# Performance work log

Measured on AMD Instinct MI355X. Metric: run time of the kernel, lower is better.

Reference implementation:

```python
import jax, jax.numpy as jnp
import numpy as np

V, E, HL, HC, B = 32000, 256, 1024, 256, 512


def setup_inputs() -> dict:
    key = jax.random.key(0)
    ks = jax.random.split(key, 10)
    s = 0.05  # small init scale, like uniform(-init_range, init_range)
    return {
        "lang_h0": jax.random.normal(ks[0], (B, HL), jnp.float32) * s,
        "ctx_h": jax.random.normal(ks[1], (B, HC), jnp.float32) * s,
        "word_emb": jax.random.normal(ks[2], (V, E), jnp.float32) * s,
        "dec_W": jax.random.normal(ks[3], (E, HL), jnp.float32) * s,
        "dec_b": jax.random.normal(ks[4], (E,), jnp.float32) * s,
        "w_ih": jax.random.normal(ks[5], (3 * HL, E + HC), jnp.float32) * s,
        "w_hh": jax.random.normal(ks[6], (3 * HL, HL), jnp.float32) * s,
        "b_ih": jax.random.normal(ks[7], (3 * HL,), jnp.float32) * s,
        "b_hh": jax.random.normal(ks[8], (3 * HL,), jnp.float32) * s,
        "inpt0": jax.random.randint(ks[9], (B,), 0, V, jnp.int32),
        "temperature": 1,
        "max_words": 100,
    }


def _gru_cell(x, h, w_ih, w_hh, b_ih, b_hh):
    # PyTorch nn.GRUCell math. x: [B, E+HC], h: [B, HL]
    gi = x @ w_ih.T + b_ih  # [B, 3*HL]
    gh = h @ w_hh.T + b_hh
    i_r, i_z, i_n = jnp.split(gi, 3, axis=-1)
    h_r, h_z, h_n = jnp.split(gh, 3, axis=-1)
    r = jax.nn.sigmoid(i_r + h_r)
    z = jax.nn.sigmoid(i_z + h_z)
    n = jnp.tanh(i_n + r * h_n)
    return (1.0 - z) * n + z * h


def reference(lang_h0, ctx_h, word_emb, dec_W, dec_b, w_ih, w_hh, b_ih, b_hh,
              inpt0, temperature, max_words):
    temp = jnp.float32(temperature)

    def step(carry, k):
        inpt, h = carry
        x = jnp.concatenate([word_emb[inpt], ctx_h], axis=1)  # [B, E+HC]
        h = _gru_cell(x, h, w_ih, w_hh, b_ih, b_hh)           # [B, HL]
        dec = h @ dec_W.T + dec_b                              # [B, E]
        logits = (dec @ word_emb.T) / temp                     # [B, V]
        # scores.sub_(max); multinomial(exp(scores)) == categorical(logits)
        out = jax.random.categorical(k, logits, axis=-1).astype(jnp.int32)
        return (out, h), (out, h)

    keys = jax.random.split(jax.random.key(1), max_words)
    (last_out, lang_h), (outs, lang_hs) = jax.lax.scan(
        step, (inpt0, lang_h0), keys)
    # final extra writer step (as in write_batch after the loop)
    x = jnp.concatenate([word_emb[last_out], ctx_h], axis=1)
    lang_h = _gru_cell(x, lang_h, w_ih, w_hh, b_ih, b_hh)
    all_lang_hs = jnp.concatenate(
        [lang_h0[None], lang_hs, lang_h[None]], axis=0)  # [T+2, B, HL]
    return outs, all_lang_hs
```

## Files before the change

### kernel.cpp

```cpp
#include <hip/hip_runtime.h>
#include <stdint.h>
#include <limits.h>

#define T_STEPS 100
#define BSZ 512
#define HL 1024
#define HC 256
#define EMB 256
#define VOC 32000
#define NCHUNK 250

typedef __attribute__((ext_vector_type(8))) short short8;
typedef __attribute__((ext_vector_type(4))) float f32x4;
typedef __attribute__((ext_vector_type(4))) unsigned short u16x4;
#define MFMA16(a, b, c) __builtin_amdgcn_mfma_f32_16x16x32_bf16(a, b, c, 0, 0, 0)

#define ACC6(acc, ah, am, al, bh, bm, bl) \
  { acc = MFMA16(ah, bh, acc); acc = MFMA16(ah, bm, acc); acc = MFMA16(am, bh, acc); \
    acc = MFMA16(ah, bl, acc); acc = MFMA16(am, bm, acc); acc = MFMA16(al, bh, acc); }

__device__ __forceinline__ void threefry2x32(uint32_t k0, uint32_t k1,
                                             uint32_t x0, uint32_t x1,
                                             uint32_t& o0, uint32_t& o1) {
  uint32_t ks2 = k0 ^ k1 ^ 0x1BD11BDAu;
  x0 += k0; x1 += k1;
#define TF_R(x, r) (((x) << (r)) | ((x) >> (32 - (r))))
#define TF_RND(r) { x0 += x1; x1 = TF_R(x1, r); x1 ^= x0; }
  TF_RND(13) TF_RND(15) TF_RND(26) TF_RND(6)
  x0 += k1; x1 += ks2 + 1u;
  TF_RND(17) TF_RND(29) TF_RND(16) TF_RND(24)
  x0 += ks2; x1 += k0 + 2u;
  TF_RND(13) TF_RND(15) TF_RND(26) TF_RND(6)
  x0 += k0; x1 += k1 + 3u;
  TF_RND(17) TF_RND(29) TF_RND(16) TF_RND(24)
  x0 += k1; x1 += ks2 + 4u;
  TF_RND(13) TF_RND(15) TF_RND(26) TF_RND(6)
  x0 += ks2; x1 += k0 + 5u;
#undef TF_RND
#undef TF_R
  o0 = x0; o1 = x1;
}

__device__ __forceinline__ float gumbel_from_u32(uint32_t bits) {
  float f = __uint_as_float((bits >> 9) | 0x3f800000u) - 1.0f;
  f = fmaxf(f, 1.17549435e-38f);
  return -logf(-logf(f));
}

__device__ __forceinline__ float read_temp(const int* p) {
  int v = *p;
  if (v >= -(1 << 24) && v <= (1 << 24)) return (float)v;
  return __int_as_float(v);
}

__device__ __forceinline__ unsigned short f2bf(float x) {
  uint32_t u = __float_as_uint(x);
  u += 0x7fffu + ((u >> 16) & 1u);
  return (unsigned short)(u >> 16);
}
__device__ __forceinline__ float bf2f(unsigned short h) {
  return __uint_as_float(((uint32_t)h) << 16);
}
__device__ __forceinline__ void split3(float x, unsigned short& h,
                                       unsigned short& m, unsigned short& l) {
  h = f2bf(x);
  float r = x - bf2f(h);
  m = f2bf(r);
  r = r - bf2f(m);
  l = f2bf(r);
}

__global__ __launch_bounds__(256) void k_split3(const float* __restrict__ src,
                                                unsigned short* __restrict__ hi,
                                                unsigned short* __restrict__ mid,
                                                unsigned short* __restrict__ lo,
                                                int n4) {
  int i = blockIdx.x * 256 + threadIdx.x;
  if (i >= n4) return;
  float4 v = ((const float4*)src)[i];
  float vv[4] = {v.x, v.y, v.z, v.w};
  u16x4 h, m, l;
#pragma unroll
  for (int j = 0; j < 4; j++) {
    unsigned short a, b, c;
    split3(vv[j], a, b, c);
    h[j] = a; m[j] = b; l[j] = c;
  }
  ((u16x4*)hi)[i] = h;
  ((u16x4*)mid)[i] = m;
  ((u16x4*)lo)[i] = l;
}

__global__ __launch_bounds__(256) void k_init(const float* __restrict__ lang_h0,
                                              const int* __restrict__ inpt0,
                                              uint32_t* __restrict__ keys,
                                              int* __restrict__ cur_tok,
                                              float* __restrict__ H0) {
  int idx = blockIdx.x * 256 + threadIdx.x;
  if (idx < T_STEPS) {
    uint32_t o0, o1;
    threefry2x32(0u, 1u, 0u, (uint32_t)idx, o0, o1);
    keys[2 * idx] = o0; keys[2 * idx + 1] = o1;
  }
  if (idx < BSZ) cur_tok[idx] = inpt0[idx];
  if (idx < BSZ * HL) H0[idx] = lang_h0[idx];
}

__global__ __launch_bounds__(256) void k_gi(
    const float* __restrict__ emb, const float* __restrict__ ctx,
    const int* __restrict__ tok,
    const unsigned short* __restrict__ wih_h, const unsigned short* __restrict__ wih_m,
    const unsigned short* __restrict__ wih_l,
    const float* __restrict__ b_ih, float* __restrict__ GI) {
  int tid = threadIdx.x;
  int wave = tid >> 6, lane = tid & 63;
  int ml = lane & 15, quad = lane >> 4;
  int n0 = blockIdx.x * 64;
  int bA = blockIdx.y * 64 + wave * 16 + ml;
  int myt = tok[bA];
  f32x4 acc[4];
#pragma unroll
  for (int tn = 0; tn < 4; tn++) acc[tn] = (f32x4){0.f, 0.f, 0.f, 0.f};

  for (int k0 = 0; k0 < 512; k0 += 32) {
    int k = k0 + quad * 8;
    const float* src = (k < 256) ? (emb + (size_t)myt * 256 + k)
                                 : (ctx + (size_t)bA * 256 + (k - 256));
    float4 x0 = *(const float4*)src;
    float4 x1 = *(const float4*)(src + 4);
    float xf[8] = {x0.x, x0.y, x0.z, x0.w, x1.x, x1.y, x1.z, x1.w};
    short8 ah, am_, al;
#pragma unroll
    for (int j = 0; j < 8; j++) {
      unsigned short a, b, c;
      split3(xf[j], a, b, c);
      ah[j] = (short)a; am_[j] = (short)b; al[j] = (short)c;
    }
#pragma unroll
    for (int tn = 0; tn < 4; tn++) {
      int n = n0 + tn * 16 + ml;
      size_t off = (size_t)n * 512 + k;
      short8 bh = *(const short8*)(wih_h + off);
      short8 bm = *(const short8*)(wih_m + off);
      short8 bl = *(const short8*)(wih_l + off);
      ACC6(acc[tn], ah, am_, al, bh, bm, bl);
    }
  }
  int brow = blockIdx.y * 64 + wave * 16 + quad * 4;
#pragma unroll
  for (int tn = 0; tn < 4; tn++) {
    int n = n0 + tn * 16 + ml;
    float bias = b_ih[n];
#pragma unroll
    for (int reg = 0; reg < 4; reg++)
      GI[(size_t)(brow + reg) * 3072 + n] = acc[tn][reg] + bias;
  }
}

__global__ __launch_bounds__(128) void k_gru(const float* __restrict__ Hin,
                                             const float* __restrict__ w_hh,
                                             const float* __restrict__ b_hh,
                                             const float* __restrict__ GI,
                                             float* __restrict__ Hout) {
  __shared__ __align__(16) float Ah[32][68];
  __shared__ __align__(16) float Wr[32][34];
  __shared__ __align__(16) float Wz[32][34];
  __shared__ __align__(16) float Wn[32][34];
  int tid = threadIdx.x;
  int ti = tid & 15;
  int tb = tid >> 4;
  int b0 = blockIdx.y * 64, i0 = blockIdx.x * 32;
  int sr = tid >> 3;
  int kq = (tid & 7) * 4;
  float acc[3][8][2] = {};

  for (int k0 = 0; k0 < 1024; k0 += 32) {
#pragma unroll
    for (int i = 0; i < 4; i++) {
      int r = sr + 16 * i;
      float4 h4 = *(const float4*)&Hin[(size_t)(b0 + r) * 1024 + k0 + kq];
      Ah[kq + 0][r] = h4.x; Ah[kq + 1][r] = h4.y; Ah[kq + 2][r] = h4.z; Ah[kq + 3][r] = h4.w;
    }
#pragma unroll
    for (int g = 0; g < 3; g++) {
      float* Wg = (g == 0 ? &Wr[0][0] : g == 1 ? &Wz[0][0] : &Wn[0][0]);
      const float* src = w_hh + (size_t)(g * 1024 + i0) * 1024;
#pragma unroll
      for (int i = 0; i < 2; i++) {
        int r = sr + 16 * i;
        float4 w4 = *(const float4*)&src[(size_t)r * 1024 + k0 + kq];
        Wg[(kq + 0) * 34 + r] = w4.x; Wg[(kq + 1) * 34 + r] = w4.y;
        Wg[(kq + 2) * 34 + r] = w4.z; Wg[(kq + 3) * 34 + r] = w4.w;
      }
    }
    __syncthreads();
#pragma unroll
    for (int kk = 0; kk < 32; kk++) {
      float4 a0 = *(float4*)&Ah[kk][tb * 8];
      float4 a1 = *(float4*)&Ah[kk][tb * 8 + 4];
      float av[8] = {a0.x, a0.y, a0.z, a0.w, a1.x, a1.y, a1.z, a1.w};
      float2 wr2 = *(float2*)&Wr[kk][ti * 2];
      float2 wz2 = *(float2*)&Wz[kk][ti * 2];
      float2 wn2 = *(float2*)&Wn[kk][ti * 2];
      float wv0[2] = {wr2.x, wr2.y};
      float wv1[2] = {wz2.x, wz2.y};
      float wv2[2] = {wn2.x, wn2.y};
#pragma unroll
      for (int bb = 0; bb < 8; bb++)
#pragma unroll
        for (int j = 0; j < 2; j++) {
          acc[0][bb][j] += av[bb] * wv0[j];
          acc[1][bb][j] += av[bb] * wv1[j];
          acc[2][bb][j] += av[bb] * wv2[j];
        }
    }
    __syncthreads();
  }
  int i = i0 + ti * 2;
  float2 bhr = *(const float2*)&b_hh[i];
  float2 bhz = *(const float2*)&b_hh[1024 + i];
  float2 bhn = *(const float2*)&b_hh[2048 + i];
  float bhrv[2] = {bhr.x, bhr.y}, bhzv[2] = {bhz.x, bhz.y}, bhnv[2] = {bhn.x, bhn.y};
#pragma unroll
  for (int bb = 0; bb < 8; bb++) {
    int b = b0 + tb * 8 + bb;
    float2 gir = *(const float2*)&GI[(size_t)b * 3072 + i];
    float2 giz = *(const float2*)&GI[(size_t)b * 3072 + 1024 + i];
    float2 gin = *(const float2*)&GI[(size_t)b * 3072 + 2048 + i];
    float2 h2 = *(const float2*)&Hin[(size_t)b * 1024 + i];
    float girv[2] = {gir.x, gir.y}, gizv[2] = {giz.x, giz.y}, ginv[2] = {gin.x, gin.y};
    float hv[2] = {h2.x, h2.y}, ov[2];
#pragma unroll
    for (int j = 0; j < 2; j++) {
      float r = 1.0f / (1.0f + expf(-(girv[j] + acc[0][bb][j] + bhrv[j])));
      float z = 1.0f / (1.0f + expf(-(gizv[j] + acc[1][bb][j] + bhzv[j])));
      float n = tanhf(ginv[j] + r * (acc[2][bb][j] + bhnv[j]));
      ov[j] = (1.0f - z) * n + z * hv[j];
    }
    float2 o; o.x = ov[0]; o.y = ov[1];
    *(float2*)&Hout[(size_t)b * 1024 + i] = o;
  }
}

__global__ __launch_bounds__(256) void k_dec(const float* __restrict__ H,
                                             const float* __restrict__ dec_W,
                                             const float* __restrict__ dec_b,
                                             unsigned short* __restrict__ dh,
                                             unsigned short* __restrict__ dm,
                                             unsigned short* __restrict__ dl) {
  __shared__ __align__(16) float As[32][20];
  __shared__ __align__(16) float Ws[32][68];
  int tid = threadIdx.x;
  int tb = tid >> 4;
  int tv = tid & 15;
  int col0 = blockIdx.x * 64, row0 = blockIdx.y * 16;
  int srw = tid >> 3;
  int kq = (tid & 7) * 4;
  float acc[4] = {};
  for (int k0 = 0; k0 < 1024; k0 += 32) {
    if (srw < 16) {
      float4 a4 = *(const float4*)&H[(size_t)(row0 + srw) * 1024 + k0 + kq];
      As[kq + 0][srw] = a4.x; As[kq + 1][srw] = a4.y; As[kq + 2][srw] = a4.z; As[kq + 3][srw] = a4.w;
    }
#pragma unroll
    for (int i = 0; i < 2; i++) {
      int r = srw + 32 * i;
      float4 w4 = *(const float4*)&dec_W[(size_t)(col0 + r) * 1024 + k0 + kq];
      Ws[kq + 0][r] = w4.x; Ws[kq + 1][r] = w4.y;
      Ws[kq + 2][r] = w4.z; Ws[kq + 3][r] = w4.w;
    }
    __syncthreads();
#pragma unroll
    for (int kk = 0; kk < 32; kk++) {
      float a = As[kk][tb];
      float4 w = *(float4*)&Ws[kk][tv * 4];
      float wv[4] = {w.x, w.y, w.z, w.w};
#pragma unroll
      for (int j = 0; j < 4; j++) acc[j] += a * wv[j];
    }
    __syncthreads();
  }
  int col = col0 + tv * 4;
  float4 b4 = *(const float4*)&dec_b[col];
  float bv[4] = {b4.x, b4.y, b4.z, b4.w};
  u16x4 h, m, l;
#pragma unroll
  for (int j = 0; j < 4; j++) {
    unsigned short a, b, c;
    split3(acc[j] + bv[j], a, b, c);
    h[j] = a; m[j] = b; l[j] = c;
  }
  size_t o = (size_t)(row0 + tb) * 256 + col;
  *(u16x4*)(dh + o) = h;
  *(u16x4*)(dm + o) = m;
  *(u16x4*)(dl + o) = l;
}

__global__ __launch_bounds__(256) void k_logits(const unsigned short* __restrict__ dh,
                                                const unsigned short* __restrict__ dm,
                                                const unsigned short* __restrict__ dl,
                                                const unsigned short* __restrict__ ebh,
                                                const unsigned short* __restrict__ ebm,
                                                const unsigned short* __restrict__ ebl,
                                                const uint32_t* __restrict__ keys,
                                                int t,
                                                const int* __restrict__ temp_ptr,
                                                float* __restrict__ pval,
                                                int* __restrict__ pidx) {
  __shared__ __align__(16) unsigned short Eh[128 * 40];
  __shared__ __align__(16) unsigned short Em[128 * 40];
  __shared__ __align__(16) unsigned short El[128 * 40];
  int tid = threadIdx.x;
  int wave = tid >> 6, lane = tid & 63;
  int ml = lane & 15, quad = lane >> 4;
  int c = blockIdx.x;
  int v0 = c * 128;
  int b0 = blockIdx.y * 128;
  f32x4 acc[2][8];
#pragma unroll
  for (int mi = 0; mi < 2; mi++)
#pragma unroll
    for (int tv = 0; tv < 8; tv++) acc[mi][tv] = (f32x4){0.f, 0.f, 0.f, 0.f};

  for (int k0 = 0; k0 < 256; k0 += 32) {
    __syncthreads();
#pragma unroll
    for (int i = 0; i < 4; i++) {
      int idx4 = tid + i * 256;
      int v = idx4 >> 3;
      int k4 = (idx4 & 7) * 4;
      size_t go = (size_t)(v0 + v) * 256 + k0 + k4;
      *(u16x4*)&Eh[v * 40 + k4] = *(const u16x4*)(ebh + go);
      *(u16x4*)&Em[v * 40 + k4] = *(const u16x4*)(ebm + go);
      *(u16x4*)&El[v * 40 + k4] = *(const u16x4*)(ebl + go);
    }
    __syncthreads();
    short8 ah[2], am_[2], al[2];
#pragma unroll
    for (int mi = 0; mi < 2; mi++) {
      int brow = b0 + wave * 32 + mi * 16 + ml;
      size_t off = (size_t)brow * 256 + k0 + quad * 8;
      ah[mi] = *(const short8*)(dh + off);
      am_[mi] = *(const short8*)(dm + off);
      al[mi] = *(const short8*)(dl + off);
    }
#pragma unroll
    for (int tv = 0; tv < 8; tv++) {
      int lo = (tv * 16 + ml) * 40 + quad * 8;
      short8 bh = *(const short8*)&Eh[lo];
      short8 bm = *(const short8*)&Em[lo];
      short8 bl = *(const short8*)&El[lo];
#pragma unroll
      for (int mi = 0; mi < 2; mi++)
        ACC6(acc[mi][tv], ah[mi], am_[mi], al[mi], bh, bm, bl);
    }
  }
  float temp = read_temp(temp_ptr);
  uint32_t kk0 = keys[2 * t], kk1 = keys[2 * t + 1];
#pragma unroll
  for (int mi = 0; mi < 2; mi++) {
    float best[4];
    int bidx[4];
#pragma unroll
    for (int reg = 0; reg < 4; reg++) { best[reg] = -3.402823466e38f; bidx[reg] = INT_MAX; }
#pragma unroll
    for (int tv = 0; tv < 8; tv++) {
      int v = v0 + tv * 16 + ml;
#pragma unroll
      for (int reg = 0; reg < 4; reg++) {
        int b = b0 + wave * 32 + mi * 16 + quad * 4 + reg;
        uint32_t o0, o1;
        threefry2x32(kk0, kk1, 0u, (uint32_t)(b * VOC + v), o0, o1);
        float s = acc[mi][tv][reg] / temp + gumbel_from_u32(o0 ^ o1);
        if (s > best[reg]) { best[reg] = s; bidx[reg] = v; }
      }
    }
#pragma unroll
    for (int off = 1; off < 16; off <<= 1) {
#pragma unroll
      for (int reg = 0; reg < 4; reg++) {
        float ov = __shfl_xor(best[reg], off, 64);
        int oi = __shfl_xor(bidx[reg], off, 64);
        if (ov > best[reg] || (ov == best[reg] && oi < bidx[reg])) {
          best[reg] = ov; bidx[reg] = oi;
        }
      }
    }
    if (ml == 0) {
#pragma unroll
      for (int reg = 0; reg < 4; reg++) {
        int b = b0 + wave * 32 + mi * 16 + quad * 4 + reg;
        pval[(size_t)b * NCHUNK + c] = best[reg];
        pidx[(size_t)b * NCHUNK + c] = bidx[reg];
      }
    }
  }
}

__global__ __launch_bounds__(256) void k_argmax_final(const float* __restrict__ pval,
                                                      const int* __restrict__ pidx,
                                                      int* __restrict__ cur_tok,
                                                      float* __restrict__ outs_t) {
  __shared__ float sv[256];
  __shared__ int si[256];
  int b = blockIdx.x, tid = threadIdx.x;
  float bv = -3.402823466e38f;
  int bi = INT_MAX;
  for (int c = tid; c < NCHUNK; c += 256) {
    float v = pval[(size_t)b * NCHUNK + c];
    int i2 = pidx[(size_t)b * NCHUNK + c];
    if (v > bv || (v == bv && i2 < bi)) { bv = v; bi = i2; }
  }
  sv[tid] = bv; si[tid] = bi;
  __syncthreads();
  for (int s = 128; s > 0; s >>= 1) {
    if (tid < s) {
      float v = sv[tid + s]; int i2 = si[tid + s];
      if (v > sv[tid] || (v == sv[tid] && i2 < si[tid])) { sv[tid] = v; si[tid] = i2; }
    }
    __syncthreads();
  }
  if (tid == 0) { cur_tok[b] = si[0]; outs_t[b] = (float)si[0]; }
}

extern "C" void kernel_launch(void* const* d_in, const int* in_sizes, int n_in,
                              void* d_out, int out_size, void* d_ws, size_t ws_size,
                              hipStream_t stream) {
  const float* lang_h0 = (const float*)d_in[0];
  const float* ctx_h   = (const float*)d_in[1];
  const float* emb     = (const float*)d_in[2];
  const float* dec_W   = (const float*)d_in[3];
  const float* dec_b   = (const float*)d_in[4];
  const float* w_ih    = (const float*)d_in[5];
  const float* w_hh    = (const float*)d_in[6];
  const float* b_ih    = (const float*)d_in[7];
  const float* b_hh    = (const float*)d_in[8];
  const int*   inpt0   = (const int*)d_in[9];
  const int*   temp_p  = (const int*)d_in[10];

  float* out = (float*)d_out;
  float* outs = out;
  float* Hbase = out + (size_t)T_STEPS * BSZ;

  uint8_t* ws = (uint8_t*)d_ws;
  uint32_t* keys = (uint32_t*)ws;
  int* cur_tok = (int*)(ws + 4096);
  unsigned short* dh = (unsigned short*)(ws + 8192);
  unsigned short* dm = dh + (size_t)BSZ * EMB;
  unsigned short* dl = dm + (size_t)BSZ * EMB;
  float* pval = (float*)(dl + (size_t)BSZ * EMB);
  int* pidx = (int*)(pval + (size_t)BSZ * NCHUNK);
  float* GI = (float*)(pidx + (size_t)BSZ * NCHUNK);
  unsigned short* wih_h = (unsigned short*)(GI + (size_t)BSZ * 3 * HL);
  unsigned short* wih_m = wih_h + (size_t)3 * HL * 512;
  unsigned short* wih_l = wih_m + (size_t)3 * HL * 512;
  unsigned short* ebh = wih_l + (size_t)3 * HL * 512;
  unsigned short* ebm = ebh + (size_t)VOC * EMB;
  unsigned short* ebl = ebm + (size_t)VOC * EMB;

  k_split3<<<(3 * HL * 512 / 4 + 255) / 256, 256, 0, stream>>>(w_ih, wih_h, wih_m, wih_l,
                                                               3 * HL * 512 / 4);
  k_split3<<<(VOC * EMB / 4 + 255) / 256, 256, 0, stream>>>(emb, ebh, ebm, ebl,
                                                            VOC * EMB / 4);
  k_init<<<(BSZ * HL) / 256, 256, 0, stream>>>(lang_h0, inpt0, keys, cur_tok, Hbase);

  for (int t = 0; t <= T_STEPS; t++) {
    const float* Hin = Hbase + (size_t)t * BSZ * HL;
    float* Hout = Hbase + (size_t)(t + 1) * BSZ * HL;
    k_gi<<<dim3(48, 8), 256, 0, stream>>>(emb, ctx_h, cur_tok,
                                          wih_h, wih_m, wih_l, b_ih, GI);
    k_gru<<<dim3(32, 8), 128, 0, stream>>>(Hin, w_hh, b_hh, GI, Hout);
    if (t == T_STEPS) break;
    k_dec<<<dim3(4, 32), 256, 0, stream>>>(Hout, dec_W, dec_b, dh, dm, dl);
    k_logits<<<dim3(NCHUNK, 4), 256, 0, stream>>>(dh, dm, dl, ebh, ebm, ebl, keys, t,
                                                  temp_p, pval, pidx);
    k_argmax_final<<<BSZ, 256, 0, stream>>>(pval, pidx, cur_tok, outs + (size_t)t * BSZ);
  }
}
```

Baseline: 29.09 ms.

## Fuse GRU input and hidden GEMMs into one split-bf16 MFMA GEMM

Concatenates w_ih and w_hh into one pre-split bf16x3 weight matrix with a separate column block for the hidden n-gate. The recurrent h@w_hh GEMM then runs on MFMA instead of the scalar FP32 shared-memory kernel. Each step now pre-splits [emb|ctx|h] into bf16 triples, runs one combined GEMM that skips zero K ranges per gate, and applies the gates in a separate pointwise kernel. This adds workspace, an extra launch and a global round-trip for the gate preactivations, and it relies on 3-way bf16 splitting to keep FP32-like accuracy.

```diff
diff --git a/kernel.cpp b/kernel.cpp
--- a/kernel.cpp
+++ b/kernel.cpp
@@ -9,6 +9,8 @@
 #define EMB 256
 #define VOC 32000
 #define NCHUNK 250
+#define KCAT 1536
+#define NCAT 4096
 
 typedef __attribute__((ext_vector_type(8))) short short8;
 typedef __attribute__((ext_vector_type(4))) float f32x4;
@@ -91,11 +93,48 @@
   ((u16x4*)lo)[i] = l;
 }
 
+__global__ __launch_bounds__(256) void k_wprep(const float* __restrict__ w_ih,
+                                               const float* __restrict__ w_hh,
+                                               unsigned short* __restrict__ wch,
+                                               unsigned short* __restrict__ wcm,
+                                               unsigned short* __restrict__ wcl) {
+  int i4 = blockIdx.x * 256 + threadIdx.x;
+  if (i4 >= NCAT * KCAT / 4) return;
+  int idx = i4 * 4;
+  int n = idx / KCAT;
+  int k = idx - n * KCAT;
+  float4 v;
+  if (k < 512) {
+    if (n < 3072) v = *(const float4*)&w_ih[(size_t)n * 512 + k];
+    else          v = (float4){0.f, 0.f, 0.f, 0.f};
+  } else {
+    int g = n >> 10;
+    if (g < 2)       v = *(const float4*)&w_hh[(size_t)n * 1024 + (k - 512)];
+    else if (g == 3) v = *(const float4*)&w_hh[(size_t)(n - 1024) * 1024 + (k - 512)];
+    else             v = (float4){0.f, 0.f, 0.f, 0.f};
+  }
+  float vv[4] = {v.x, v.y, v.z, v.w};
+  u16x4 h, m, l;
+#pragma unroll
+  for (int j = 0; j < 4; j++) {
+    unsigned short a, b, c;
+    split3(vv[j], a, b, c);
+    h[j] = a; m[j] = b; l[j] = c;
+  }
+  size_t o = (size_t)n * KCAT + k;
+  *(u16x4*)(wch + o) = h;
+  *(u16x4*)(wcm + o) = m;
+  *(u16x4*)(wcl + o) = l;
+}
+
 __global__ __launch_bounds__(256) void k_init(const float* __restrict__ lang_h0,
                                               const int* __restrict__ inpt0,
+                                              const float* __restrict__ b_ih,
+                                              const float* __restrict__ b_hh,
                                               uint32_t* __restrict__ keys,
                                               int* __restrict__ cur_tok,
-                                              float* __restrict__ H0) {
+                                              float* __restrict__ H0,
+                                              float* __restrict__ bc) {
   int idx = blockIdx.x * 256 + threadIdx.x;
   if (idx < T_STEPS) {
     uint32_t o0, o1;
@@ -103,46 +142,79 @@
     keys[2 * idx] = o0; keys[2 * idx + 1] = o1;
   }
   if (idx < BSZ) cur_tok[idx] = inpt0[idx];
+  if (idx < NCAT) {
+    int g = idx >> 10;
+    float v;
+    if (g < 2)       v = b_ih[idx] + b_hh[idx];
+    else if (g == 2) v = b_ih[idx];
+    else             v = b_hh[idx - 1024];
+    bc[idx] = v;
+  }
   if (idx < BSZ * HL) H0[idx] = lang_h0[idx];
 }
 
-__global__ __launch_bounds__(256) void k_gi(
-    const float* __restrict__ emb, const float* __restrict__ ctx,
-    const int* __restrict__ tok,
-    const unsigned short* __restrict__ wih_h, const unsigned short* __restrict__ wih_m,
-    const unsigned short* __restrict__ wih_l,
-    const float* __restrict__ b_ih, float* __restrict__ GI) {
+__global__ __launch_bounds__(256) void k_xsplit(const float* __restrict__ emb,
+                                                const float* __restrict__ ctx,
+                                                const int* __restrict__ tok,
+                                                const float* __restrict__ Hin,
+                                                unsigned short* __restrict__ xh,
+                                                unsigned short* __restrict__ xm,
+                                                unsigned short* __restrict__ xl) {
+  int i4 = blockIdx.x * 256 + threadIdx.x;
+  if (i4 >= BSZ * KCAT / 4) return;
+  int idx = i4 * 4;
+  int b = idx / KCAT;
+  int k = idx - b * KCAT;
+  const float* src;
+  if (k < 256)      src = emb + (size_t)tok[b] * 256 + k;
+  else if (k < 512) src = ctx + (size_t)b * 256 + (k - 256);
+  else              src = Hin + (size_t)b * 1024 + (k - 512);
+  float4 v = *(const float4*)src;
+  float vv[4] = {v.x, v.y, v.z, v.w};
+  u16x4 h, m, l;
+#pragma unroll
+  for (int j = 0; j < 4; j++) {
+    unsigned short a, bb, c;
+    split3(vv[j], a, bb, c);
+    h[j] = a; m[j] = bb; l[j] = c;
+  }
+  size_t o = (size_t)b * KCAT + k;
+  *(u16x4*)(xh + o) = h;
+  *(u16x4*)(xm + o) = m;
+  *(u16x4*)(xl + o) = l;
+}
+
+__global__ __launch_bounds__(256) void k_big(
+    const unsigned short* __restrict__ xh, const unsigned short* __restrict__ xm,
+    const unsigned short* __restrict__ xl,
+    const unsigned short* __restrict__ wch, const unsigned short* __restrict__ wcm,
+    const unsigned short* __restrict__ wcl,
+    const float* __restrict__ bc, float* __restrict__ Gp) {
   int tid = threadIdx.x;
   int wave = tid >> 6, lane = tid & 63;
   int ml = lane & 15, quad = lane >> 4;
   int n0 = blockIdx.x * 64;
+  int gate = n0 >> 10;
+  int kbeg = (gate == 3) ? 512 : 0;
+  int kend = (gate == 2) ? 512 : KCAT;
   int bA = blockIdx.y * 64 + wave * 16 + ml;
-  int myt = tok[bA];
   f32x4 acc[4];
 #pragma unroll
   for (int tn = 0; tn < 4; tn++) acc[tn] = (f32x4){0.f, 0.f, 0.f, 0.f};
 
-  for (int k0 = 0; k0 < 512; k0 += 32) {
+  for (int k0 = kbeg; k0 < kend; k0 += 32) {
     int k = k0 + quad * 8;
-    const float* src = (k < 256) ? (emb + (size_t)myt * 256 + k)
-                                 : (ctx + (size_t)bA * 256 + (k - 256));
-    float4 x0 = *(const float4*)src;
-    float4 x1 = *(const float4*)(src + 4);
-    float xf[8] = {x0.x, x0.y, x0.z, x0.w, x1.x, x1.y, x1.z, x1.w};
-    short8 ah, am_, al;
-#pragma unroll
-    for (int j = 0; j < 8; j++) {
-      unsigned short a, b, c;
-      split3(xf[j], a, b, c);
-      ah[j] = (short)a; am_[j] = (short)b; al[j] = (short)c;
-    }
+    size_t aoff = (size_t)bA * KCAT + k;
+    short8 ah = *(const short8*)(xh + aoff);
+    short8 am_ = *(const short8*)(xm + aoff);
+    short8 al = *(const short8*)(xl + aoff);
 #pragma unroll
     for (int tn = 0; tn < 4; tn++) {
       int n = n0 + tn * 16 + ml;
-      size_t off = (size_t)n * 512 + k;
-      short8 bh = *(const short8*)(wih_h + off);
-      short8 bm = *(const short8*)(wih_m + off);
-      short8 bl = *(const short8*)(wih_l + off);
+      size_t off = (size_t)n * KCAT + k;
+      short8 bh = *(const short8*)(wch + off);
+      short8 bm = *(const short8*)(wcm + off);
+      short8 bl = *(const short8*)(wcl + off);
       ACC6(acc[tn], ah, am_, al, bh, bm, bl);
     }
   }
@@ -150,96 +222,41 @@
 #pragma unroll
   for (int tn = 0; tn < 4; tn++) {
     int n = n0 + tn * 16 + ml;
-    float bias = b_ih[n];
+    float bias = bc[n];
 #pragma unroll
     for (int reg = 0; reg < 4; reg++)
-      GI[(size_t)(brow + reg) * 3072 + n] = acc[tn][reg] + bias;
-  }
-}
-
-__global__ __launch_bounds__(128) void k_gru(const float* __restrict__ Hin,
-                                             const float* __restrict__ w_hh,
-                                             const float* __restrict__ b_hh,
-                                             const float* __restrict__ GI,
-                                             float* __restrict__ Hout) {
-  __shared__ __align__(16) float Ah[32][68];
-  __shared__ __align__(16) float Wr[32][34];
-  __shared__ __align__(16) float Wz[32][34];
-  __shared__ __align__(16) float Wn[32][34];
-  int tid = threadIdx.x;
-  int ti = tid & 15;
-  int tb = tid >> 4;
-  int b0 = blockIdx.y * 64, i0 = blockIdx.x * 32;
-  int sr = tid >> 3;
-  int kq = (tid & 7) * 4;
-  float acc[3][8][2] = {};
-
-  for (int k0 = 0; k0 < 1024; k0 += 32) {
-#pragma unroll
-    for (int i = 0; i < 4; i++) {
-      int r = sr + 16 * i;
-      float4 h4 = *(const float4*)&Hin[(size_t)(b0 + r) * 1024 + k0 + kq];
-      Ah[kq + 0][r] = h4.x; Ah[kq + 1][r] = h4.y; Ah[kq + 2][r] = h4.z; Ah[kq + 3][r] = h4.w;
-    }
-#pragma unroll
-    for (int g = 0; g < 3; g++) {
-      float* Wg = (g == 0 ? &Wr[0][0] : g == 1 ? &Wz[0][0] : &Wn[0][0]);
-      const float* src = w_hh + (size_t)(g * 1024 + i0) * 1024;
-#pragma unroll
-      for (int i = 0; i < 2; i++) {
-        int r = sr + 16 * i;
-        float4 w4 = *(const float4*)&src[(size_t)r * 1024 + k0 + kq];
-        Wg[(kq + 0) * 34 + r] = w4.x; Wg[(kq + 1) * 34 + r] = w4.y;
-        Wg[(kq + 2) * 34 + r] = w4.z; Wg[(kq + 3) * 34 + r] = w4.w;
-      }
-    }
-    __syncthreads();
-#pragma unroll
-    for (int kk = 0; kk < 32; kk++) {
-      float4 a0 = *(float4*)&Ah[kk][tb * 8];
-      float4 a1 = *(float4*)&Ah[kk][tb * 8 + 4];
-      float av[8] = {a0.x, a0.y, a0.z, a0.w, a1.x, a1.y, a1.z, a1.w};
-      float2 wr2 = *(float2*)&Wr[kk][ti * 2];
-      float2 wz2 = *(float2*)&Wz[kk][ti * 2];
-      float2 wn2 = *(float2*)&Wn[kk][ti * 2];
-      float wv0[2] = {wr2.x, wr2.y};
-      float wv1[2] = {wz2.x, wz2.y};
-      float wv2[2] = {wn2.x, wn2.y};
-#pragma unroll
-      for (int bb = 0; bb < 8; bb++)
-#pragma unroll
-        for (int j = 0; j < 2; j++) {
-          acc[0][bb][j] += av[bb] * wv0[j];
-          acc[1][bb][j] += av[bb] * wv1[j];
-          acc[2][bb][j] += av[bb] * wv2[j];
-        }
-    }
-    __syncthreads();
-  }
-  int i = i0 + ti * 2;
-  float2 bhr = *(const float2*)&b_hh[i];
-  float2 bhz = *(const float2*)&b_hh[1024 + i];
-  float2 bhn = *(const float2*)&b_hh[2048 + i];
-  float bhrv[2] = {bhr.x, bhr.y}, bhzv[2] = {bhz.x, bhz.y}, bhnv[2] = {bhn.x, bhn.y};
-#pragma unroll
-  for (int bb = 0; bb < 8; bb++) {
-    int b = b0 + tb * 8 + bb;
-    float2 gir = *(const float2*)&GI[(size_t)b * 3072 + i];
-    float2 giz = *(const float2*)&GI[(size_t)b * 3072 + 1024 + i];
-    float2 gin = *(const float2*)&GI[(size_t)b * 3072 + 2048 + i];
-    float2 h2 = *(const float2*)&Hin[(size_t)b * 1024 + i];
-    float girv[2] = {gir.x, gir.y}, gizv[2] = {giz.x, giz.y}, ginv[2] = {gin.x, gin.y};
-    float hv[2] = {h2.x, h2.y}, ov[2];
-#pragma unroll
-    for (int j = 0; j < 2; j++) {
-      float r = 1.0f / (1.0f + expf(-(girv[j] + acc[0][bb][j] + bhrv[j])));
-      float z = 1.0f / (1.0f + expf(-(gizv[j] + acc[1][bb][j] + bhzv[j])));
-      float n = tanhf(ginv[j] + r * (acc[2][bb][j] + bhnv[j]));
-      ov[j] = (1.0f - z) * n + z * hv[j];
-    }
-    float2 o; o.x = ov[0]; o.y = ov[1];
-    *(float2*)&Hout[(size_t)b * 1024 + i] = o;
-  }
+      Gp[(size_t)(brow + reg) * NCAT + n] = acc[tn][reg] + bias;
+  }
+}
+
+__global__ __launch_bounds__(256) void k_point(const float* __restrict__ Gp,
+                                               const float* __restrict__ Hin,
+                                               float* __restrict__ Hout) {
+  int i4 = blockIdx.x * 256 + threadIdx.x;
+  if (i4 >= BSZ * HL / 4) return;
+  int idx = i4 * 4;
+  int b = idx >> 10, i = idx & 1023;
+  const float* g = Gp + (size_t)b * NCAT;
+  float4 gr = *(const float4*)(g + i);
+  float4 gz = *(const float4*)(g + 1024 + i);
+  float4 gn = *(const float4*)(g + 2048 + i);
+  float4 gh = *(const float4*)(g + 3072 + i);
+  float4 h4 = *(const float4*)(Hin + (size_t)b * 1024 + i);
+  float grv[4] = {gr.x, gr.y, gr.z, gr.w};
+  float gzv[4] = {gz.x, gz.y, gz.z, gz.w};
+  float gnv[4] = {gn.x, gn.y, gn.z, gn.w};
+  float ghv[4] = {gh.x, gh.y, gh.z, gh.w};
+  float hv[4] = {h4.x, h4.y, h4.z, h4.w};
+  float ov[4];
+#pragma unroll
+  for (int j = 0; j < 4; j++) {
+    float r = 1.0f / (1.0f + expf(-grv[j]));
+    float z = 1.0f / (1.0f + expf(-gzv[j]));
+    float n = tanhf(gnv[j] + r * ghv[j]);
+    ov[j] = (1.0f - z) * n + z * hv[j];
+  }
+  float4 o; o.x = ov[0]; o.y = ov[1]; o.z = ov[2]; o.w = ov[3];
+  *(float4*)&Hout[(size_t)b * 1024 + i] = o;
 }
 
 __global__ __launch_bounds__(256) void k_dec(const float* __restrict__ H,
@@ -450,26 +467,32 @@
   unsigned short* dl = dm + (size_t)BSZ * EMB;
   float* pval = (float*)(dl + (size_t)BSZ * EMB);
   int* pidx = (int*)(pval + (size_t)BSZ * NCHUNK);
-  float* GI = (float*)(pidx + (size_t)BSZ * NCHUNK);
-  unsigned short* wih_h = (unsigned short*)(GI + (size_t)BSZ * 3 * HL);
-  unsigned short* wih_m = wih_h + (size_t)3 * HL * 512;
-  unsigned short* wih_l = wih_m + (size_t)3 * HL * 512;
-  unsigned short* ebh = wih_l + (size_t)3 * HL * 512;
+  float* Gp = (float*)(pidx + (size_t)BSZ * NCHUNK);
+  unsigned short* xh = (unsigned short*)(Gp + (size_t)BSZ * NCAT);
+  unsigned short* xm = xh + (size_t)BSZ * KCAT;
+  unsigned short* xl = xm + (size_t)BSZ * KCAT;
+  unsigned short* wch = xl + (size_t)BSZ * KCAT;
+  unsigned short* wcm = wch + (size_t)NCAT * KCAT;
+  unsigned short* wcl = wcm + (size_t)NCAT * KCAT;
+  float* bc = (float*)(wcl + (size_t)NCAT * KCAT);
+  unsigned short* ebh = (unsigned short*)(bc + NCAT);
   unsigned short* ebm = ebh + (size_t)VOC * EMB;
   unsigned short* ebl = ebm + (size_t)VOC * EMB;
 
-  k_split3<<<(3 * HL * 512 / 4 + 255) / 256, 256, 0, stream>>>(w_ih, wih_h, wih_m, wih_l,
-                                                               3 * HL * 512 / 4);
+  k_wprep<<<(NCAT * KCAT / 4 + 255) / 256, 256, 0, stream>>>(w_ih, w_hh, wch, wcm, wcl);
   k_split3<<<(VOC * EMB / 4 + 255) / 256, 256, 0, stream>>>(emb, ebh, ebm, ebl,
                                                             VOC * EMB / 4);
-  k_init<<<(BSZ * HL) / 256, 256, 0, stream>>>(lang_h0, inpt0, keys, cur_tok, Hbase);
+  k_init<<<(BSZ * HL) / 256, 256, 0, stream>>>(lang_h0, inpt0, b_ih, b_hh,
+                                               keys, cur_tok, Hbase, bc);
 
   for (int t = 0; t <= T_STEPS; t++) {
     const float* Hin = Hbase + (size_t)t * BSZ * HL;
     float* Hout = Hbase + (size_t)(t + 1) * BSZ * HL;
-    k_gi<<<dim3(48, 8), 256, 0, stream>>>(emb, ctx_h, cur_tok,
-                                          wih_h, wih_m, wih_l, b_ih, GI);
-    k_gru<<<dim3(32, 8), 128, 0, stream>>>(Hin, w_hh, b_hh, GI, Hout);
+    k_xsplit<<<(BSZ * KCAT / 4 + 255) / 256, 256, 0, stream>>>(emb, ctx_h, cur_tok,
+                                                               Hin, xh, xm, xl);
+    k_big<<<dim3(NCAT / 64, BSZ / 64), 256, 0, stream>>>(xh, xm, xl, wch, wcm, wcl,
+                                                         bc, Gp);
+    k_point<<<(BSZ * HL / 4 + 255) / 256, 256, 0, stream>>>(Gp, Hin, Hout);
     if (t == T_STEPS) break;
     k_dec<<<dim3(4, 32), 256, 0, stream>>>(Hout, dec_W, dec_b, dh, dm, dl);
     k_logits<<<dim3(NCHUNK, 4), 256, 0, stream>>>(dh, dm, dl, ebh, ebm, ebl, keys, t,
```

Result: slower. 31.24 ms (+7.4%).

## Fuse argmax into logits via packed atomicMax, presplit embeddings, retile GRU

Applied to the files above, without the earlier changes.

Removes the per-step argmax reduction kernel. Each logits block now folds its chunk maximum into a packed 64-bit key with atomicMax, and the next gi kernel unpacks the token and writes it to the output. The gi kernel also reads the pre-split bf16 embedding and context tables (context is split once up front) instead of splitting on the fly. The GRU kernel is retiled to 32 batch rows per block to double the block count. This saves a launch and the partial-buffer traffic per step, at the cost of atomic contention and an extra write in the decoder kernel to reset the packed keys.

```diff
diff --git a/kernel.cpp b/kernel.cpp
--- a/kernel.cpp
+++ b/kernel.cpp
@@ -70,6 +70,10 @@
   l = f2bf(r);
 }
 
+__device__ __forceinline__ int unpack_tok(unsigned long long pk) {
+  return (int)(0xFFFFFFFFu - (uint32_t)(pk & 0xFFFFFFFFull));
+}
+
 __global__ __launch_bounds__(256) void k_split3(const float* __restrict__ src,
                                                 unsigned short* __restrict__ hi,
                                                 unsigned short* __restrict__ mid,
@@ -94,7 +98,7 @@
 __global__ __launch_bounds__(256) void k_init(const float* __restrict__ lang_h0,
                                               const int* __restrict__ inpt0,
                                               uint32_t* __restrict__ keys,
-                                              int* __restrict__ cur_tok,
+                                              unsigned long long* __restrict__ packed,
                                               float* __restrict__ H0) {
   int idx = blockIdx.x * 256 + threadIdx.x;
   if (idx < T_STEPS) {
@@ -102,39 +106,46 @@
     threefry2x32(0u, 1u, 0u, (uint32_t)idx, o0, o1);
     keys[2 * idx] = o0; keys[2 * idx + 1] = o1;
   }
-  if (idx < BSZ) cur_tok[idx] = inpt0[idx];
+  if (idx < BSZ)
+    packed[idx] = (unsigned long long)(0xFFFFFFFFu - (uint32_t)inpt0[idx]);
   if (idx < BSZ * HL) H0[idx] = lang_h0[idx];
 }
 
 __global__ __launch_bounds__(256) void k_gi(
-    const float* __restrict__ emb, const float* __restrict__ ctx,
-    const int* __restrict__ tok,
+    const unsigned short* __restrict__ ebh, const unsigned short* __restrict__ ebm,
+    const unsigned short* __restrict__ ebl,
+    const unsigned short* __restrict__ cxh, const unsigned short* __restrict__ cxm,
+    const unsigned short* __restrict__ cxl,
+    const unsigned long long* __restrict__ packed,
     const unsigned short* __restrict__ wih_h, const unsigned short* __restrict__ wih_m,
     const unsigned short* __restrict__ wih_l,
-    const float* __restrict__ b_ih, float* __restrict__ GI) {
+    const float* __restrict__ b_ih, float* __restrict__ GI,
+    int t, float* __restrict__ outs) {
   int tid = threadIdx.x;
   int wave = tid >> 6, lane = tid & 63;
   int ml = lane & 15, quad = lane >> 4;
   int n0 = blockIdx.x * 64;
   int bA = blockIdx.y * 64 + wave * 16 + ml;
-  int myt = tok[bA];
+  int myt = unpack_tok(packed[bA]);
+  if (blockIdx.x == 0 && quad == 0 && t > 0)
+    outs[(size_t)(t - 1) * BSZ + bA] = (float)myt;
   f32x4 acc[4];
 #pragma unroll
   for (int tn = 0; tn < 4; tn++) acc[tn] = (f32x4){0.f, 0.f, 0.f, 0.f};
 
   for (int k0 = 0; k0 < 512; k0 += 32) {
     int k = k0 + quad * 8;
-    const float* src = (k < 256) ? (emb + (size_t)myt * 256 + k)
-                                 : (ctx + (size_t)bA * 256 + (k - 256));
-    float4 x0 = *(const float4*)src;
-    float4 x1 = *(const float4*)(src + 4);
-    float xf[8] = {x0.x, x0.y, x0.z, x0.w, x1.x, x1.y, x1.z, x1.w};
     short8 ah, am_, al;
-#pragma unroll
-    for (int j = 0; j < 8; j++) {
-      unsigned short a, b, c;
-      split3(xf[j], a, b, c);
-      ah[j] = (short)a; am_[j] = (short)b; al[j] = (short)c;
+    if (k < 256) {
+      size_t eo = (size_t)myt * 256 + k;
+      ah = *(const short8*)(ebh + eo);
+      am_ = *(const short8*)(ebm + eo);
+      al = *(const short8*)(ebl + eo);
+    } else {
+      size_t co = (size_t)bA * 256 + (k - 256);
+      ah = *(const short8*)(cxh + co);
+      am_ = *(const short8*)(cxm + co);
+      al = *(const short8*)(cxl + co);
     }
 #pragma unroll
     for (int tn = 0; tn < 4; tn++) {
@@ -162,21 +173,21 @@
                                              const float* __restrict__ b_hh,
                                              const float* __restrict__ GI,
                                              float* __restrict__ Hout) {
-  __shared__ __align__(16) float Ah[32][68];
+  __shared__ __align__(16) float Ah[32][36];
   __shared__ __align__(16) float Wr[32][34];
   __shared__ __align__(16) float Wz[32][34];
   __shared__ __align__(16) float Wn[32][34];
   int tid = threadIdx.x;
   int ti = tid & 15;
   int tb = tid >> 4;
-  int b0 = blockIdx.y * 64, i0 = blockIdx.x * 32;
+  int b0 = blockIdx.y * 32, i0 = blockIdx.x * 32;
   int sr = tid >> 3;
   int kq = (tid & 7) * 4;
-  float acc[3][8][2] = {};
+  float acc[3][4][2] = {};
 
   for (int k0 = 0; k0 < 1024; k0 += 32) {
 #pragma unroll
-    for (int i = 0; i < 4; i++) {
+    for (int i = 0; i < 2; i++) {
       int r = sr + 16 * i;
       float4 h4 = *(const float4*)&Hin[(size_t)(b0 + r) * 1024 + k0 + kq];
       Ah[kq + 0][r] = h4.x; Ah[kq + 1][r] = h4.y; Ah[kq + 2][r] = h4.z; Ah[kq + 3][r] = h4.w;
@@ -196,9 +207,8 @@
     __syncthreads();
 #pragma unroll
     for (int kk = 0; kk < 32; kk++) {
-      float4 a0 = *(float4*)&Ah[kk][tb * 8];
-      float4 a1 = *(float4*)&Ah[kk][tb * 8 + 4];
-      float av[8] = {a0.x, a0.y, a0.z, a0.w, a1.x, a1.y, a1.z, a1.w};
+      float4 a0 = *(float4*)&Ah[kk][tb * 4];
+      float av[4] = {a0.x, a0.y, a0.z, a0.w};
       float2 wr2 = *(float2*)&Wr[kk][ti * 2];
       float2 wz2 = *(float2*)&Wz[kk][ti * 2];
       float2 wn2 = *(float2*)&Wn[kk][ti * 2];
@@ -206,7 +216,7 @@
       float wv1[2] = {wz2.x, wz2.y};
       float wv2[2] = {wn2.x, wn2.y};
 #pragma unroll
-      for (int bb = 0; bb < 8; bb++)
+      for (int bb = 0; bb < 4; bb++)
 #pragma unroll
         for (int j = 0; j < 2; j++) {
           acc[0][bb][j] += av[bb] * wv0[j];
@@ -222,8 +232,8 @@
   float2 bhn = *(const float2*)&b_hh[2048 + i];
   float bhrv[2] = {bhr.x, bhr.y}, bhzv[2] = {bhz.x, bhz.y}, bhnv[2] = {bhn.x, bhn.y};
 #pragma unroll
-  for (int bb = 0; bb < 8; bb++) {
-    int b = b0 + tb * 8 + bb;
+  for (int bb = 0; bb < 4; bb++) {
+    int b = b0 + tb * 4 + bb;
     float2 gir = *(const float2*)&GI[(size_t)b * 3072 + i];
     float2 giz = *(const float2*)&GI[(size_t)b * 3072 + 1024 + i];
     float2 gin = *(const float2*)&GI[(size_t)b * 3072 + 2048 + i];
@@ -247,13 +257,15 @@
                                              const float* __restrict__ dec_b,
                                              unsigned short* __restrict__ dh,
                                              unsigned short* __restrict__ dm,
-                                             unsigned short* __restrict__ dl) {
+                                             unsigned short* __restrict__ dl,
+                                             unsigned long long* __restrict__ packed) {
   __shared__ __align__(16) float As[32][20];
   __shared__ __align__(16) float Ws[32][68];
   int tid = threadIdx.x;
   int tb = tid >> 4;
   int tv = tid & 15;
   int col0 = blockIdx.x * 64, row0 = blockIdx.y * 16;
+  if (blockIdx.x == 0 && tid < 16) packed[row0 + tid] = 0ull;
   int srw = tid >> 3;
   int kq = (tid & 7) * 4;
   float acc[4] = {};
@@ -305,8 +317,7 @@
                                                 const uint32_t* __restrict__ keys,
                                                 int t,
                                                 const int* __restrict__ temp_ptr,
-                                                float* __restrict__ pval,
-                                                int* __restrict__ pidx) {
+                                                unsigned long long* __restrict__ packed) {
   __shared__ __align__(16) unsigned short Eh[128 * 40];
   __shared__ __align__(16) unsigned short Em[128 * 40];
   __shared__ __align__(16) unsigned short El[128 * 40];
@@ -390,37 +401,14 @@
 #pragma unroll
       for (int reg = 0; reg < 4; reg++) {
         int b = b0 + wave * 32 + mi * 16 + quad * 4 + reg;
-        pval[(size_t)b * NCHUNK + c] = best[reg];
-        pidx[(size_t)b * NCHUNK + c] = bidx[reg];
+        uint32_t u = __float_as_uint(best[reg]);
+        uint32_t mp = (u & 0x80000000u) ? ~u : (u | 0x80000000u);
+        unsigned long long key = ((unsigned long long)mp << 32) |
+                                 (unsigned long long)(0xFFFFFFFFu - (uint32_t)bidx[reg]);
+        atomicMax(&packed[b], key);
       }
     }
   }
-}
-
-__global__ __launch_bounds__(256) void k_argmax_final(const float* __restrict__ pval,
-                                                      const int* __restrict__ pidx,
-                                                      int* __restrict__ cur_tok,
-                                                      float* __restrict__ outs_t) {
-  __shared__ float sv[256];
-  __shared__ int si[256];
-  int b = blockIdx.x, tid = threadIdx.x;
-  float bv = -3.402823466e38f;
-  int bi = INT_MAX;
-  for (int c = tid; c < NCHUNK; c += 256) {
-    float v = pval[(size_t)b * NCHUNK + c];
-    int i2 = pidx[(size_t)b * NCHUNK + c];
-    if (v > bv || (v == bv && i2 < bi)) { bv = v; bi = i2; }
-  }
-  sv[tid] = bv; si[tid] = bi;
-  __syncthreads();
-  for (int s = 128; s > 0; s >>= 1) {
-    if (tid < s) {
-      float v = sv[tid + s]; int i2 = si[tid + s];
-      if (v > sv[tid] || (v == sv[tid] && i2 < si[tid])) { sv[tid] = v; si[tid] = i2; }
-    }
-    __syncthreads();
-  }
-  if (tid == 0) { cur_tok[b] = si[0]; outs_t[b] = (float)si[0]; }
 }
 
 extern "C" void kernel_launch(void* const* d_in, const int* in_sizes, int n_in,
@@ -444,36 +432,38 @@
 
   uint8_t* ws = (uint8_t*)d_ws;
   uint32_t* keys = (uint32_t*)ws;
-  int* cur_tok = (int*)(ws + 4096);
-  unsigned short* dh = (unsigned short*)(ws + 8192);
+  unsigned long long* packed = (unsigned long long*)(ws + 4096);
+  unsigned short* dh = (unsigned short*)(ws + 16384);
   unsigned short* dm = dh + (size_t)BSZ * EMB;
   unsigned short* dl = dm + (size_t)BSZ * EMB;
-  float* pval = (float*)(dl + (size_t)BSZ * EMB);
-  int* pidx = (int*)(pval + (size_t)BSZ * NCHUNK);
-  float* GI = (float*)(pidx + (size_t)BSZ * NCHUNK);
+  float* GI = (float*)(dl + (size_t)BSZ * EMB);
   unsigned short* wih_h = (unsigned short*)(GI + (size_t)BSZ * 3 * HL);
   unsigned short* wih_m = wih_h + (size_t)3 * HL * 512;
   unsigned short* wih_l = wih_m + (size_t)3 * HL * 512;
   unsigned short* ebh = wih_l + (size_t)3 * HL * 512;
   unsigned short* ebm = ebh + (size_t)VOC * EMB;
   unsigned short* ebl = ebm + (size_t)VOC * EMB;
+  unsigned short* cxh = ebl + (size_t)VOC * EMB;
+  unsigned short* cxm = cxh + (size_t)BSZ * HC;
+  unsigned short* cxl = cxm + (size_t)BSZ * HC;
 
   k_split3<<<(3 * HL * 512 / 4 + 255) / 256, 256, 0, stream>>>(w_ih, wih_h, wih_m, wih_l,
                                                                3 * HL * 512 / 4);
   k_split3<<<(VOC * EMB / 4 + 255) / 256, 256, 0, stream>>>(emb, ebh, ebm, ebl,
                                                             VOC * EMB / 4);
-  k_init<<<(BSZ * HL) / 256, 256, 0, stream>>>(lang_h0, inpt0, keys, cur_tok, Hbase);
+  k_split3<<<(BSZ * HC / 4 + 255) / 256, 256, 0, stream>>>(ctx_h, cxh, cxm, cxl,
+                                                           BSZ * HC / 4);
+  k_init<<<(BSZ * HL) / 256, 256, 0, stream>>>(lang_h0, inpt0, keys, packed, Hbase);
 
   for (int t = 0; t <= T_STEPS; t++) {
     const float* Hin = Hbase + (size_t)t * BSZ * HL;
     float* Hout = Hbase + (size_t)(t + 1) * BSZ * HL;
-    k_gi<<<dim3(48, 8), 256, 0, stream>>>(emb, ctx_h, cur_tok,
-                                          wih_h, wih_m, wih_l, b_ih, GI);
-    k_gru<<<dim3(32, 8), 128, 0, stream>>>(Hin, w_hh, b_hh, GI, Hout);
+    k_gi<<<dim3(48, 8), 256, 0, stream>>>(ebh, ebm, ebl, cxh, cxm, cxl, packed,
+                                          wih_h, wih_m, wih_l, b_ih, GI, t, outs);
+    k_gru<<<dim3(32, 16), 128, 0, stream>>>(Hin, w_hh, b_hh, GI, Hout);
     if (t == T_STEPS) break;
-    k_dec<<<dim3(4, 32), 256, 0, stream>>>(Hout, dec_W, dec_b, dh, dm, dl);
+    k_dec<<<dim3(4, 32), 256, 0, stream>>>(Hout, dec_W, dec_b, dh, dm, dl, packed);
     k_logits<<<dim3(NCHUNK, 4), 256, 0, stream>>>(dh, dm, dl, ebh, ebm, ebl, keys, t,
-                                                  temp_p, pval, pidx);
-    k_argmax_final<<<BSZ, 256, 0, stream>>>(pval, pidx, cur_tok, outs + (size_t)t * BSZ);
-  }
-}
+                                                  temp_p, packed);
+  }
+}
```

After: 29.84 ms. 2.6% more time.
